# Performance work log

Hardware: AMD Instinct MI355X
Metric: run time of the kernel (lower is better)

Reference implementation:

```python
import jax, jax.numpy as jnp
import numpy as np

H = 1024        # hidden_size
NH = 16         # num_attention_heads
DH = H // NH    # head dim = 64
I = 4096        # intermediate_size
E = 8           # moe_num_experts
B, S = 2, 2048
EPS = 1e-12


def _ln(x, g, b):
    mu = jnp.mean(x, axis=-1, keepdims=True)
    var = jnp.mean(jnp.square(x - mu), axis=-1, keepdims=True)
    return (x - mu) * jax.lax.rsqrt(var + EPS) * g + b


def setup_inputs() -> dict:
    key = jax.random.key(0)
    ks = jax.random.split(key, 16)
    std = 0.02
    p = {
        "hidden_states": jax.random.normal(ks[0], (B, S, H), jnp.float32),
        "Wq": jax.random.normal(ks[1], (H, H), jnp.float32) * std,
        "bq": jnp.zeros((H,), jnp.float32),
        "Wk": jax.random.normal(ks[2], (H, H), jnp.float32) * std,
        "bk": jnp.zeros((H,), jnp.float32),
        "Wv": jax.random.normal(ks[3], (H, H), jnp.float32) * std,
        "bv": jnp.zeros((H,), jnp.float32),
        "Wao": jax.random.normal(ks[4], (H, H), jnp.float32) * std,
        "bao": jnp.zeros((H,), jnp.float32),
        "ln1_g": jnp.ones((H,), jnp.float32),
        "ln1_b": jnp.zeros((H,), jnp.float32),
        "router_w": jax.random.normal(ks[5], (H, E), jnp.float32) * std,
        "We": jax.random.normal(ks[6], (E, H, I), jnp.float32) * std,
        "be": jnp.zeros((E, I), jnp.float32),
        "Wo": jax.random.normal(ks[7], (I, H), jnp.float32) * std,
        "bo": jnp.zeros((H,), jnp.float32),
        "ln2_g": jnp.ones((H,), jnp.float32),
        "ln2_b": jnp.zeros((H,), jnp.float32),
    }
    return p


def reference(hidden_states, Wq, bq, Wk, bk, Wv, bv, Wao, bao, ln1_g, ln1_b,
              router_w, We, be, Wo, bo, ln2_g, ln2_b):
    x = hidden_states  # [B,S,H]

    def heads(t):  # [B,S,H] -> [B,NH,S,DH]
        return t.reshape(B, S, NH, DH).transpose(0, 2, 1, 3)

    q = heads(x @ Wq + bq)
    k = heads(x @ Wk + bk)
    v = heads(x @ Wv + bv)
    scores = jnp.einsum("bhqd,bhkd->bhqk", q, k) / jnp.sqrt(jnp.float32(DH))
    probs = jax.nn.softmax(scores, axis=-1)
    ctx = jnp.einsum("bhqk,bhkd->bhqd", probs, v)
    ctx = ctx.transpose(0, 2, 1, 3).reshape(B, S, H)
    attn_out = _ln(ctx @ Wao + bao + x, ln1_g, ln1_b)  # BertSelfOutput

    # ---- MoE FFN: top-1 routing, per-expert GELU MLP, shared output proj ----
    flat = attn_out.reshape(-1, H)              # [N,H]
    logits = flat @ router_w                    # [N,E]
    idx = jnp.argmax(logits, axis=-1)           # top-1 of softmax == argmax of logits
    inter = jnp.zeros((flat.shape[0], I), flat.dtype)
    for e in range(E):  # small fixed expert count
        h_e = jax.nn.gelu(flat @ We[e] + be[e], approximate=False)
        inter = jnp.where((idx == e)[:, None], h_e, inter)
    inter = inter.reshape(B, S, I)
    out = _ln(inter @ Wo + bo + attn_out, ln2_g, ln2_b)  # BertOutput
    return out
```

## Files before the change

kernel.cpp:

```cpp
#include <hip/hip_runtime.h>
#include <hip/hip_bf16.h>
#include <cstdint>

#define H_  1024
#define NH_ 16
#define DH_ 64
#define I_  4096
#define E_  8
#define B_  2
#define S_  2048
#define N_  4096
#define QKVLD 3072
#define LN_EPS 1e-12f

typedef __attribute__((ext_vector_type(4))) float f4;
typedef __attribute__((ext_vector_type(8))) short s8v;
typedef unsigned int u32;

__device__ __forceinline__ float bf2f(unsigned short u) {
  union { unsigned int i; float f; } c; c.i = ((unsigned int)u) << 16; return c.f;
}
__device__ __forceinline__ unsigned short f2bf(float f) {
  __hip_bfloat16 h = __float2bfloat16(f);
  return *reinterpret_cast<unsigned short*>(&h);
}
__device__ __forceinline__ u32 pack_bf2(float a, float b) {
  return (u32)f2bf(a) | ((u32)f2bf(b) << 16);
}
__device__ __forceinline__ float gelu_f(float x) {
  return 0.5f * x * (1.0f + erff(x * 0.70710678118f));
}
__device__ __forceinline__ void gload16(const void* g, void* l) {
  __builtin_amdgcn_global_load_lds(
      (const __attribute__((address_space(1))) void*)g,
      (__attribute__((address_space(3))) void*)l, 16, 0, 0);
}

__global__ __launch_bounds__(256) void cvt_bf16_kernel(
    const float* __restrict__ in, ushort* __restrict__ out, int n8)
{
  const int t = blockIdx.x * 256 + threadIdx.x;
  if (t >= n8) return;
  const f4 x0 = *(const f4*)(in + (size_t)t * 8);
  const f4 x1 = *(const f4*)(in + (size_t)t * 8 + 4);
  s8v o;
#pragma unroll
  for (int j = 0; j < 4; ++j) { o[j] = (short)f2bf(x0[j]); o[4 + j] = (short)f2bf(x1[j]); }
  *(s8v*)(out + (size_t)t * 8) = o;
}

__global__ __launch_bounds__(256) void transpose_cvt_kernel(
    const float* __restrict__ in, ushort* __restrict__ out, int R, int C)
{
  __shared__ float Ls[64][68];
  const size_t zo = (size_t)blockIdx.z * (size_t)R * C;
  const int bx = blockIdx.x << 6;
  const int by = blockIdx.y << 6;
  const int tid = threadIdx.x;
  const int lr = tid >> 4, lc4 = (tid & 15) << 2;
  const float* ip = in + zo + (size_t)(by + lr) * C + bx + lc4;
#pragma unroll
  for (int i = 0; i < 4; ++i)
    *(f4*)&Ls[lr + (i << 4)][lc4] = *(const f4*)(ip + (size_t)(i << 4) * C);
  __syncthreads();
  const int oc = tid >> 2, seg = (tid & 3) << 4;
  ushort* op = out + zo + (size_t)(bx + oc) * R + by + seg;
  s8v v0, v1;
#pragma unroll
  for (int j = 0; j < 8; ++j) {
    v0[j] = (short)f2bf(Ls[seg + j][oc]);
    v1[j] = (short)f2bf(Ls[seg + 8 + j][oc]);
  }
  *(s8v*)op = v0;
  *(s8v*)(op + 8) = v1;
}

__global__ void concat3_kernel(const float* a, const float* b, const float* c,
                               float* __restrict__ o)
{
  const int t = blockIdx.x * 256 + threadIdx.x;
  if (t < 1024) o[t] = a[t];
  else if (t < 2048) o[t] = b[t - 1024];
  else o[t] = c[t - 2048];
}

__global__ __launch_bounds__(256) void gather_kernel(
    const ushort* __restrict__ X, const int* __restrict__ lists,
    ushort* __restrict__ Xg)
{
  const int r = (blockIdx.x << 1) + (threadIdx.x >> 7);
  const int c = (threadIdx.x & 127) << 3;
  const int tok = lists[r];
  *(s8v*)&Xg[(size_t)r * H_ + c] = *(const s8v*)&X[(size_t)tok * H_ + c];
}

template <bool BF16OUT, int KSPLIT>
__global__ __launch_bounds__(256, 3) void gemm_mfma_kernel(
    const ushort* __restrict__ A, const ushort* __restrict__ Bt,
    const float* __restrict__ bias, void* __restrict__ Cout,
    const int M, const int N, const int K)
{
  __shared__ __align__(16) ushort Asm[3][4][128][8];
  __shared__ __align__(16) ushort Bsm[3][4][128][8];
  const int tid = threadIdx.x;
  const int w = tid >> 6, l = tid & 63;
  const int lq = l & 15, g = l >> 4;
  const int wm = w >> 1, wn = w & 1;
  const int nbx = N >> 7;
  const int nwg = nbx * (M >> 7);
  int id = blockIdx.y * nbx + blockIdx.x;
  id = (id & 7) * (nwg >> 3) + (id >> 3);
  const int m0 = (id / nbx) << 7, n0 = (id % nbx) << 7;
  const int Kspan = K / KSPLIT;
  const int kbase = (KSPLIT > 1) ? blockIdx.z * Kspan : 0;

  const ushort* a0 = A + (size_t)(m0 + l) * K + kbase + (w << 3);
  const ushort* a1 = a0 + (size_t)64 * K;
  const ushort* b0 = Bt + (size_t)(n0 + l) * K + kbase + (w << 3);
  const ushort* b1 = b0 + (size_t)64 * K;

  f4 acc[4][4] = {};
  const int nt = Kspan >> 5;
#define STAGE_G(tt, buf)                                   \
  { const int kt_ = (tt) << 5;                             \
    gload16(a0 + kt_, &Asm[buf][w][0][0]);                 \
    gload16(a1 + kt_, &Asm[buf][w][64][0]);                \
    gload16(b0 + kt_, &Bsm[buf][w][0][0]);                 \
    gload16(b1 + kt_, &Bsm[buf][w][64][0]); }
  STAGE_G(0, 0);
  STAGE_G(1, 1);
  int cur = 0, nxt2 = 2;
  for (int t = 0; t < nt; ++t) {
    if (t + 1 < nt) { asm volatile("s_waitcnt vmcnt(4)" ::: "memory"); }
    else            { asm volatile("s_waitcnt vmcnt(0)" ::: "memory"); }
    __builtin_amdgcn_s_barrier();
    __builtin_amdgcn_sched_barrier(0);
    if (t + 2 < nt) STAGE_G(t + 2, nxt2);
    s8v af[4], bfv[4];
#pragma unroll
    for (int mi = 0; mi < 4; ++mi)
      af[mi] = *(const s8v*)&Asm[cur][g][(wm << 6) + (mi << 4) + lq][0];
#pragma unroll
    for (int ni = 0; ni < 4; ++ni)
      bfv[ni] = *(const s8v*)&Bsm[cur][g][(wn << 6) + (ni << 4) + lq][0];
    asm volatile("s_waitcnt lgkmcnt(0)" ::: "memory");
    __builtin_amdgcn_sched_barrier(0);
#pragma unroll
    for (int mi = 0; mi < 4; ++mi)
#pragma unroll
      for (int ni = 0; ni < 4; ++ni)
        acc[mi][ni] = __builtin_amdgcn_mfma_f32_16x16x32_bf16(af[mi], bfv[ni], acc[mi][ni], 0, 0, 0);
    cur = (cur == 2) ? 0 : cur + 1;
    nxt2 = (nxt2 == 2) ? 0 : nxt2 + 1;
  }
#undef STAGE_G
  if constexpr (BF16OUT) {
    ushort* st = (ushort*)Asm + (size_t)w * (16 * 72);
    float bs[4];
#pragma unroll
    for (int ni = 0; ni < 4; ++ni) bs[ni] = bias[n0 + (wn << 6) + (ni << 4) + lq];
#pragma unroll
    for (int mi = 0; mi < 4; ++mi) {
#pragma unroll
      for (int ni = 0; ni < 4; ++ni)
#pragma unroll
        for (int r = 0; r < 4; ++r)
          st[((g << 2) + r) * 72 + (ni << 4) + lq] = f2bf(acc[mi][ni][r] + bs[ni]);
#pragma unroll
      for (int q2 = 0; q2 < 2; ++q2) {
        const int r16 = l & 15, ch = (l >> 4) + (q2 << 2);
        const s8v vv = *(const s8v*)&st[r16 * 72 + (ch << 3)];
        *(s8v*)&((ushort*)Cout)[(size_t)(m0 + (wm << 6) + (mi << 4) + r16) * N
                                + n0 + (wn << 6) + (ch << 3)] = vv;
      }
    }
  } else {
    float* outf = (float*)Cout + (size_t)blockIdx.z * M * N;
#pragma unroll
    for (int ni = 0; ni < 4; ++ni) {
      const int col = n0 + (wn << 6) + (ni << 4) + lq;
      const float bs = (KSPLIT == 1 || blockIdx.z == 0) ? bias[col] : 0.f;
#pragma unroll
      for (int mi = 0; mi < 4; ++mi) {
        const int row = m0 + (wm << 6) + (mi << 4) + (g << 2);
#pragma unroll
        for (int r = 0; r < 4; ++r)
          outf[(size_t)(row + r) * N + col] = acc[mi][ni][r] + bs;
      }
    }
  }
}

__global__ __launch_bounds__(256, 3) void moe_mfma_kernel(
    const ushort* __restrict__ Xg, const ushort* __restrict__ WeT,
    const float* __restrict__ be, const int* __restrict__ lists,
    const int* __restrict__ offs, const int* __restrict__ cnt,
    const int* __restrict__ tb, ushort* __restrict__ inter)
{
  __shared__ __align__(16) ushort Asm[3][4][128][8];
  __shared__ __align__(16) ushort Bsm[3][4][128][8];
  __shared__ int tokL[128];
  const int by = blockIdx.y;
  if (by >= tb[E_]) return;
  int e = 0;
#pragma unroll
  for (int t = 1; t < E_; ++t) if (by >= tb[t]) e = t;
  const int rt = by - tb[e];
  const int base = offs[e] + (rt << 7);
  const int nrows = cnt[e] - (rt << 7);
  const int tid = threadIdx.x;
  if (tid < 128) tokL[tid] = (tid < nrows) ? lists[base + tid] : -1;
  __syncthreads();
  const int w = tid >> 6, l = tid & 63;
  const int lq = l & 15, g = l >> 4;
  const int wm = w >> 1, wn = w & 1;
  const int n0 = blockIdx.x << 7;
  const int r0 = min(base + l, N_ - 1);
  const int r1 = min(base + 64 + l, N_ - 1);
  const ushort* a0 = Xg + (size_t)r0 * H_ + (w << 3);
  const ushort* a1 = Xg + (size_t)r1 * H_ + (w << 3);
  const ushort* Wp = WeT + (size_t)e * I_ * H_;
  const ushort* b0 = Wp + (size_t)(n0 + l) * H_ + (w << 3);
  const ushort* b1 = b0 + (size_t)64 * H_;

  f4 acc[4][4] = {};
#define STAGE_M(tt, buf)                                   \
  { const int kt_ = (tt) << 5;                             \
    gload16(a0 + kt_, &Asm[buf][w][0][0]);                 \
    gload16(a1 + kt_, &Asm[buf][w][64][0]);                \
    gload16(b0 + kt_, &Bsm[buf][w][0][0]);                 \
    gload16(b1 + kt_, &Bsm[buf][w][64][0]); }
  STAGE_M(0, 0);
  STAGE_M(1, 1);
  int cur = 0, nxt2 = 2;
  for (int t = 0; t < 32; ++t) {
    if (t + 1 < 32) { asm volatile("s_waitcnt vmcnt(4)" ::: "memory"); }
    else            { asm volatile("s_waitcnt vmcnt(0)" ::: "memory"); }
    __builtin_amdgcn_s_barrier();
    __builtin_amdgcn_sched_barrier(0);
    if (t + 2 < 32) STAGE_M(t + 2, nxt2);
    s8v af[4], bfv[4];
#pragma unroll
    for (int mi = 0; mi < 4; ++mi)
      af[mi] = *(const s8v*)&Asm[cur][g][(wm << 6) + (mi << 4) + lq][0];
#pragma unroll
    for (int ni = 0; ni < 4; ++ni)
      bfv[ni] = *(const s8v*)&Bsm[cur][g][(wn << 6) + (ni << 4) + lq][0];
    asm volatile("s_waitcnt lgkmcnt(0)" ::: "memory");
    __builtin_amdgcn_sched_barrier(0);
#pragma unroll
    for (int mi = 0; mi < 4; ++mi)
#pragma unroll
      for (int ni = 0; ni < 4; ++ni)
        acc[mi][ni] = __builtin_amdgcn_mfma_f32_16x16x32_bf16(af[mi], bfv[ni], acc[mi][ni], 0, 0, 0);
    cur = (cur == 2) ? 0 : cur + 1;
    nxt2 = (nxt2 == 2) ? 0 : nxt2 + 1;
  }
#undef STAGE_M
  {
    ushort* st = (ushort*)Asm + (size_t)w * (16 * 72);
    float bs[4];
#pragma unroll
    for (int ni = 0; ni < 4; ++ni) bs[ni] = be[(size_t)e * I_ + n0 + (wn << 6) + (ni << 4) + lq];
#pragma unroll
    for (int mi = 0; mi < 4; ++mi) {
#pragma unroll
      for (int ni = 0; ni < 4; ++ni)
#pragma unroll
        for (int r = 0; r < 4; ++r)
          st[((g << 2) + r) * 72 + (ni << 4) + lq] = f2bf(gelu_f(acc[mi][ni][r] + bs[ni]));
#pragma unroll
      for (int q2 = 0; q2 < 2; ++q2) {
        const int r16 = l & 15, ch = (l >> 4) + (q2 << 2);
        const int tok = tokL[(wm << 6) + (mi << 4) + r16];
        if (tok >= 0) {
          const s8v vv = *(const s8v*)&st[r16 * 72 + (ch << 3)];
          *(s8v*)&inter[(size_t)tok * I_ + n0 + (wn << 6) + (ch << 3)] = vv;
        }
      }
    }
  }
}

__global__ __launch_bounds__(256) void attn_mfma_kernel(
    const ushort* __restrict__ qkv, ushort* __restrict__ ctx)
{
  __shared__ __align__(16) ushort Ks[64 * 72];
  __shared__ __align__(16) ushort Vr[64 * 72];
  __shared__ __align__(16) ushort Vt[64 * 72];
  __shared__ __align__(16) ushort Ps[4][16 * 72];
  const int bid0 = blockIdx.x;
  const int bid  = ((bid0 & 7) << 7) + (bid0 >> 3);
  const int bh = bid >> 5, qt = bid & 31;
  const int b = bh >> 4, h = bh & 15;
  const int tid = threadIdx.x, w = tid >> 6, l = tid & 63;
  const int lq = l & 15, g = l >> 4;
  const size_t bS = (size_t)b * S_;
  const ushort* qb = qkv + bS * QKVLD + h * DH_;
  const ushort* kb = qb + 1024;
  const ushort* vb = qb + 2048;

  s8v qf0, qf1;
  {
    const ushort* qp = qb + (size_t)(qt * 64 + w * 16 + lq) * QKVLD;
    qf0 = *(const s8v*)(qp + (g << 3));
    qf1 = *(const s8v*)(qp + 32 + (g << 3));
  }

  f4 o0 = {0,0,0,0}, o1 = {0,0,0,0}, o2 = {0,0,0,0}, o3 = {0,0,0,0};
  float mrun = -3.0e38f, lrun = 0.f;

  const int skey = tid >> 2;
  const int sd   = (tid & 3) << 4;

  s8v kr0, kr1, vr0, vr1;
#define ALOAD(t_) {                                                        \
    const ushort* kp_ = kb + (size_t)((t_) * 64 + skey) * QKVLD + sd;      \
    kr0 = *(const s8v*)kp_; kr1 = *(const s8v*)(kp_ + 8);                  \
    const ushort* vp_ = vb + (size_t)((t_) * 64 + skey) * QKVLD + sd;      \
    vr0 = *(const s8v*)vp_; vr1 = *(const s8v*)(vp_ + 8); }
#define AWRITE() {                                                         \
    *(s8v*)&Ks[skey * 72 + sd]     = kr0;                                  \
    *(s8v*)&Ks[skey * 72 + sd + 8] = kr1;                                  \
    *(s8v*)&Vr[skey * 72 + sd]     = vr0;                                  \
    *(s8v*)&Vr[skey * 72 + sd + 8] = vr1; }

  ALOAD(0); AWRITE();
  ALOAD(1);

  for (int kt = 0; kt < 32; ++kt) {
    asm volatile("s_waitcnt lgkmcnt(0)" ::: "memory");
    __builtin_amdgcn_sched_barrier(0);
    __builtin_amdgcn_s_barrier();
    __builtin_amdgcn_sched_barrier(0);

    {
      s8v t0, t1;
#pragma unroll
      for (int j = 0; j < 8; ++j) {
        t0[j] = (short)Vr[(w * 16 + j) * 72 + l];
        t1[j] = (short)Vr[(w * 16 + 8 + j) * 72 + l];
      }
      *(s8v*)&Vt[l * 72 + w * 16]     = t0;
      *(s8v*)&Vt[l * 72 + w * 16 + 8] = t1;
    }

    float s[16];
    __builtin_amdgcn_s_setprio(1);
#pragma unroll
    for (int st = 0; st < 4; ++st) {
      f4 acc = {0, 0, 0, 0};
      const s8v ka0 = *(const s8v*)&Ks[(st * 16 + lq) * 72 + (g << 3)];
      const s8v ka1 = *(const s8v*)&Ks[(st * 16 + lq) * 72 + 32 + (g << 3)];
      acc = __builtin_amdgcn_mfma_f32_16x16x32_bf16(ka0, qf0, acc, 0, 0, 0);
      acc = __builtin_amdgcn_mfma_f32_16x16x32_bf16(ka1, qf1, acc, 0, 0, 0);
      s[st * 4 + 0] = acc[0] * 0.125f; s[st * 4 + 1] = acc[1] * 0.125f;
      s[st * 4 + 2] = acc[2] * 0.125f; s[st * 4 + 3] = acc[3] * 0.125f;
    }
    __builtin_amdgcn_s_setprio(0);

    float tmax = s[0];
// ... 56 lines not shown
  for (int r = 0; r < 4; ++r) {
    const float li = __shfl(inv, g * 4 + r);
    ushort* op = ctx + (bS + (size_t)(qt * 64 + w * 16 + g * 4 + r)) * H_ + h * DH_ + lq;
    op[0]  = f2bf(o0[r] * li);
    op[16] = f2bf(o1[r] * li);
    op[32] = f2bf(o2[r] * li);
    op[48] = f2bf(o3[r] * li);
  }
}

template <int P>
__global__ __launch_bounds__(256) void add_ln_kernel(
    const float* __restrict__ a, const float* __restrict__ r,
    const float* __restrict__ g, const float* __restrict__ bta,
    float* __restrict__ out, ushort* __restrict__ ob)
{
  const int row = blockIdx.x, tid = threadIdx.x;
  const size_t base = (size_t)row * H_;
  const float4 xr = *(const float4*)(r + base + (tid << 2));
  float4 x = xr;
#pragma unroll
  for (int pp = 0; pp < P; ++pp) {
    const float4 xa = *(const float4*)(a + (size_t)pp * N_ * H_ + base + (tid << 2));
    x.x += xa.x; x.y += xa.y; x.z += xa.z; x.w += xa.w;
  }
  float s  = x.x + x.y + x.z + x.w;
  float ss = x.x * x.x + x.y * x.y + x.z * x.z + x.w * x.w;
#pragma unroll
  for (int off = 1; off < 64; off <<= 1) { s += __shfl_xor(s, off); ss += __shfl_xor(ss, off); }
  __shared__ float red[8];
  const int w = tid >> 6, ln = tid & 63;
  if (ln == 0) { red[w] = s; red[4 + w] = ss; }
  __syncthreads();
  const float S  = red[0] + red[1] + red[2] + red[3];
  const float SS = red[4] + red[5] + red[6] + red[7];
  const float mu  = S * (1.f / 1024.f);
  const float var = fmaxf(SS * (1.f / 1024.f) - mu * mu, 0.f);
  const float inv = rsqrtf(var + LN_EPS);
  const float4 gg = *(const float4*)&g[tid << 2];
  const float4 bb = *(const float4*)&bta[tid << 2];
  float4 y;
  y.x = (x.x - mu) * inv * gg.x + bb.x;
  y.y = (x.y - mu) * inv * gg.y + bb.y;
  y.z = (x.z - mu) * inv * gg.z + bb.z;
  y.w = (x.w - mu) * inv * gg.w + bb.w;
  *(float4*)&out[base + (tid << 2)] = y;
  if (ob) {
    ushort4 u;
    u.x = f2bf(y.x); u.y = f2bf(y.y); u.z = f2bf(y.z); u.w = f2bf(y.w);
    *(ushort4*)&ob[base + (tid << 2)] = u;
  }
}

__global__ __launch_bounds__(64) void router_kernel(
    const float* __restrict__ x, const float* __restrict__ rw,
    int* __restrict__ idx, int* __restrict__ cnt)
{
  const int t = blockIdx.x, lane = threadIdx.x;
  float acc[8] = {0.f};
  for (int c = 0; c < H_; c += 64) {
    const float xv = x[(size_t)t * H_ + c + lane];
    const float* wr = rw + (size_t)(c + lane) * E_;
    const float4 w0 = *(const float4*)wr;
    const float4 w1 = *(const float4*)(wr + 4);
    acc[0] += xv * w0.x; acc[1] += xv * w0.y; acc[2] += xv * w0.z; acc[3] += xv * w0.w;
    acc[4] += xv * w1.x; acc[5] += xv * w1.y; acc[6] += xv * w1.z; acc[7] += xv * w1.w;
  }
#pragma unroll
  for (int e = 0; e < E_; ++e) {
    float s = acc[e];
#pragma unroll
    for (int off = 1; off < 64; off <<= 1) s += __shfl_xor(s, off);
    acc[e] = s;
  }
  if (lane == 0) {
    int be_ = 0; float bv = acc[0];
#pragma unroll
    for (int e = 1; e < E_; ++e) if (acc[e] > bv) { bv = acc[e]; be_ = e; }
    idx[t] = be_;
    atomicAdd(&cnt[be_], 1);
  }
}

__global__ void init_kernel(int* cnt) { if (threadIdx.x < E_) cnt[threadIdx.x] = 0; }

__global__ void scan_kernel(const int* __restrict__ cnt, int* __restrict__ offs,
                            int* __restrict__ cursor, int* __restrict__ tb)
{
  int o = 0, tt = 0;
  for (int e = 0; e < E_; ++e) {
    offs[e] = o; cursor[e] = o; tb[e] = tt;
    o += cnt[e]; tt += (cnt[e] + 127) >> 7;
  }
  tb[E_] = tt;
}

__global__ __launch_bounds__(256) void scatter_kernel(
    const int* __restrict__ idx, int* __restrict__ cursor, int* __restrict__ lists)
{
  const int t = blockIdx.x * 256 + threadIdx.x;
  if (t < N_) {
    const int e = idx[t];
    const int p = atomicAdd(&cursor[e], 1);
    lists[p] = t;
  }
}

extern "C" void kernel_launch(void* const* d_in, const int* in_sizes, int n_in,
                              void* d_out, int out_size, void* d_ws, size_t ws_size,
                              hipStream_t stream) {
  const float* x   = (const float*)d_in[0];
  const float* Wq  = (const float*)d_in[1];
  const float* bq  = (const float*)d_in[2];
  const float* Wk  = (const float*)d_in[3];
  const float* bk  = (const float*)d_in[4];
  const float* Wv  = (const float*)d_in[5];
  const float* bv  = (const float*)d_in[6];
  const float* Wao = (const float*)d_in[7];
  const float* bao = (const float*)d_in[8];
  const float* g1  = (const float*)d_in[9];
  const float* b1  = (const float*)d_in[10];
  const float* rw  = (const float*)d_in[11];
  const float* We  = (const float*)d_in[12];
  const float* be  = (const float*)d_in[13];
  const float* Wo  = (const float*)d_in[14];
  const float* bo  = (const float*)d_in[15];
  const float* g2  = (const float*)d_in[16];
  const float* b2  = (const float*)d_in[17];
  float* out = (float*)d_out;

  char* p = (char*)d_ws;
  int* idx    = (int*)p; p += (size_t)N_ * 4;
  int* cnt    = (int*)p; p += 8 * 4;
  int* offs   = (int*)p; p += 8 * 4;
  int* cursor = (int*)p; p += 8 * 4;
  int* tb     = (int*)p; p += 16 * 4;
  int* lists  = (int*)p; p += (size_t)N_ * 4;
  p = (char*)(((uintptr_t)p + 255) & ~(uintptr_t)255);
  const size_t NH = (size_t)N_ * H_;
  ushort* xb     = (ushort*)p; p += NH * 2;
  ushort* qkvb   = (ushort*)p;
  float*  woPart = (float*)p;  p += (size_t)N_ * QKVLD * 2;
  ushort* ctxb   = (ushort*)p; p += NH * 2;
  float*  attn   = (float*)p;  p += NH * 4;
  ushort* attnb  = (ushort*)p; p += NH * 2;
  ushort* interb = (ushort*)p;
  float*  aoPart = (float*)p;  p += (size_t)N_ * I_ * 2;
  ushort* WqkvT  = (ushort*)p; p += (size_t)QKVLD * H_ * 2;
  ushort* WaoT   = (ushort*)p; p += (size_t)H_ * H_ * 2;
  ushort* WoT    = (ushort*)p; p += (size_t)H_ * I_ * 2;
  ushort* WeT    = (ushort*)p; p += (size_t)E_ * I_ * H_ * 2;
  float*  bqkv   = (float*)p;  p += QKVLD * 4;
  ushort* Xg     = xb;

  const dim3 blk(256);

  init_kernel<<<1, 64, 0, stream>>>(cnt);
  cvt_bf16_kernel<<<(N_ * H_ / 8 + 255) / 256, blk, 0, stream>>>(x, xb, N_ * H_ / 8);
  concat3_kernel<<<QKVLD / 256, blk, 0, stream>>>(bq, bk, bv, bqkv);
  transpose_cvt_kernel<<<dim3(16, 16, 1), blk, 0, stream>>>(Wq, WqkvT, H_, H_);
  transpose_cvt_kernel<<<dim3(16, 16, 1), blk, 0, stream>>>(Wk, WqkvT + (size_t)1024 * H_, H_, H_);
  transpose_cvt_kernel<<<dim3(16, 16, 1), blk, 0, stream>>>(Wv, WqkvT + (size_t)2048 * H_, H_, H_);
  transpose_cvt_kernel<<<dim3(16, 16, 1), blk, 0, stream>>>(Wao, WaoT, H_, H_);
  transpose_cvt_kernel<<<dim3(16, 64, 1), blk, 0, stream>>>(Wo, WoT, I_, H_);
  transpose_cvt_kernel<<<dim3(64, 16, 8), blk, 0, stream>>>(We, WeT, H_, I_);

  gemm_mfma_kernel<true, 1><<<dim3(QKVLD / 128, N_ / 128), blk, 0, stream>>>(
      xb, WqkvT, bqkv, qkvb, N_, QKVLD, H_);
  attn_mfma_kernel<<<1024, blk, 0, stream>>>(qkvb, ctxb);
  gemm_mfma_kernel<false, 2><<<dim3(H_ / 128, N_ / 128, 2), blk, 0, stream>>>(
      ctxb, WaoT, bao, aoPart, N_, H_, H_);
  add_ln_kernel<2><<<N_, blk, 0, stream>>>(aoPart, x, g1, b1, attn, attnb);
  router_kernel<<<N_, 64, 0, stream>>>(attn, rw, idx, cnt);
  scan_kernel<<<1, 1, 0, stream>>>(cnt, offs, cursor, tb);
  scatter_kernel<<<N_ / 256, blk, 0, stream>>>(idx, cursor, lists);
  gather_kernel<<<N_ / 2, blk, 0, stream>>>(attnb, lists, Xg);
  moe_mfma_kernel<<<dim3(I_ / 128, N_ / 128 + E_), blk, 0, stream>>>(
      Xg, WeT, be, lists, offs, cnt, tb, interb);
  gemm_mfma_kernel<false, 2><<<dim3(H_ / 128, N_ / 128, 2), blk, 0, stream>>>(
      interb, WoT, bo, woPart, N_, H_, I_);
  add_ln_kernel<2><<<N_, blk, 0, stream>>>(woPart, attn, g2, b2, out, (ushort*)nullptr);
}
```

Before: 509.8 us.

## Use 256x256 tiles with 512-thread blocks for QKV and MoE expert GEMMs

Measured after the change: 506.2 us. About the same (-0.7%).

```diff
diff --git a/kernel.cpp b/kernel.cpp
--- a/kernel.cpp
+++ b/kernel.cpp
@@ -92,6 +92,185 @@
   const int c = (threadIdx.x & 127) << 3;
   const int tok = lists[r];
   *(s8v*)&Xg[(size_t)r * H_ + c] = *(const s8v*)&X[(size_t)tok * H_ + c];
+}
+
+__global__ __launch_bounds__(512, 2) void gemm256_bf16_kernel(
+    const ushort* __restrict__ A, const ushort* __restrict__ Bt,
+    const float* __restrict__ bias, ushort* __restrict__ Cout,
+    const int M, const int N, const int K)
+{
+  __shared__ __align__(16) ushort Asm[3][4][256][8];
+  __shared__ __align__(16) ushort Bsm[3][4][256][8];
+  const int tid = threadIdx.x, w = tid >> 6, l = tid & 63;
+  const int lq = l & 15, g = l >> 4;
+  const int wm = w >> 2, wn = w & 3;
+  const int nbx = N >> 8;
+  const int nwg = nbx * (M >> 8);
+  int id = blockIdx.y * nbx + blockIdx.x;
+  id = (id & 7) * (nwg >> 3) + (id >> 3);
+  const int m0 = (id / nbx) << 8, n0 = (id % nbx) << 8;
+
+  const bool isB = (w >= 4);
+  const int ks = w & 3;
+  const ushort* gb = isB ? (Bt + (size_t)(n0 + l) * K + (ks << 3))
+                         : (A + (size_t)(m0 + l) * K + (ks << 3));
+  const ushort* p0 = gb;
+  const ushort* p1 = gb + (size_t)64 * K;
+  const ushort* p2 = gb + (size_t)128 * K;
+  const ushort* p3 = gb + (size_t)192 * K;
+
+  f4 acc[8][4] = {};
+  const int nt = K >> 5;
+#define STG(tt, buf) { const int kt_ = (tt) << 5;                          \
+    ushort* d = isB ? &Bsm[buf][ks][0][0] : &Asm[buf][ks][0][0];           \
+    gload16(p0 + kt_, d);          gload16(p1 + kt_, d + 64 * 8);          \
+    gload16(p2 + kt_, d + 128 * 8); gload16(p3 + kt_, d + 192 * 8); }
+  STG(0, 0);
+  STG(1, 1);
+  int cur = 0, nxt2 = 2;
+  for (int t = 0; t < nt; ++t) {
+    if (t + 1 < nt) { asm volatile("s_waitcnt vmcnt(4)" ::: "memory"); }
+    else            { asm volatile("s_waitcnt vmcnt(0)" ::: "memory"); }
+    __builtin_amdgcn_s_barrier();
+    __builtin_amdgcn_sched_barrier(0);
+    if (t + 2 < nt) STG(t + 2, nxt2);
+    s8v af[8], bfv[4];
+#pragma unroll
+    for (int mi = 0; mi < 8; ++mi)
+      af[mi] = *(const s8v*)&Asm[cur][g][(wm << 7) + (mi << 4) + lq][0];
+#pragma unroll
+    for (int ni = 0; ni < 4; ++ni)
+      bfv[ni] = *(const s8v*)&Bsm[cur][g][(wn << 6) + (ni << 4) + lq][0];
+    asm volatile("s_waitcnt lgkmcnt(0)" ::: "memory");
+    __builtin_amdgcn_sched_barrier(0);
+#pragma unroll
+    for (int mi = 0; mi < 8; ++mi)
+#pragma unroll
+      for (int ni = 0; ni < 4; ++ni)
+        acc[mi][ni] = __builtin_amdgcn_mfma_f32_16x16x32_bf16(af[mi], bfv[ni], acc[mi][ni], 0, 0, 0);
+    cur = (cur == 2) ? 0 : cur + 1;
+    nxt2 = (nxt2 == 2) ? 0 : nxt2 + 1;
+  }
+#undef STG
+  __syncthreads();
+  ushort* st = (ushort*)Asm + (size_t)w * (16 * 72);
+  float bs[4];
+#pragma unroll
+  for (int ni = 0; ni < 4; ++ni) bs[ni] = bias[n0 + (wn << 6) + (ni << 4) + lq];
+#pragma unroll
+  for (int mi = 0; mi < 8; ++mi) {
+#pragma unroll
+    for (int ni = 0; ni < 4; ++ni)
+#pragma unroll
+      for (int r = 0; r < 4; ++r)
+        st[((g << 2) + r) * 72 + (ni << 4) + lq] = f2bf(acc[mi][ni][r] + bs[ni]);
+#pragma unroll
+    for (int q2 = 0; q2 < 2; ++q2) {
+      const int r16 = l & 15, ch = (l >> 4) + (q2 << 2);
+      const s8v vv = *(const s8v*)&st[r16 * 72 + (ch << 3)];
+      *(s8v*)&Cout[(size_t)(m0 + (wm << 7) + (mi << 4) + r16) * N
+                   + n0 + (wn << 6) + (ch << 3)] = vv;
+    }
+  }
+}
+
+__global__ __launch_bounds__(512, 2) void moe256_mfma_kernel(
+    const ushort* __restrict__ Xg, const ushort* __restrict__ WeT,
+    const float* __restrict__ be, const int* __restrict__ lists,
+    const int* __restrict__ offs, const int* __restrict__ cnt,
+    const int* __restrict__ tb, ushort* __restrict__ inter)
+{
+  __shared__ __align__(16) ushort Asm[3][4][256][8];
+  __shared__ __align__(16) ushort Bsm[3][4][256][8];
+  __shared__ int tokL[256];
+  const int by = blockIdx.y;
+  if (by >= tb[E_]) return;
+  int e = 0;
+#pragma unroll
+  for (int t = 1; t < E_; ++t) if (by >= tb[t]) e = t;
+  const int rt = by - tb[e];
+  const int base = offs[e] + (rt << 8);
+  const int nrows = cnt[e] - (rt << 8);
+  const int tid = threadIdx.x;
+  if (tid < 256) tokL[tid] = (tid < nrows) ? lists[base + tid] : -1;
+  __syncthreads();
+  const int w = tid >> 6, l = tid & 63;
+  const int lq = l & 15, g = l >> 4;
+  const int wm = w >> 2, wn = w & 3;
+  const int n0 = blockIdx.x << 8;
+
+  const bool isB = (w >= 4);
+  const int ks = w & 3;
+  const ushort* Wp = WeT + (size_t)e * I_ * H_;
+  const ushort* p0;
+  const ushort* p1;
+  const ushort* p2;
+  const ushort* p3;
+  if (isB) {
+    const ushort* gb = Wp + (size_t)(n0 + l) * H_ + (ks << 3);
+    p0 = gb; p1 = gb + (size_t)64 * H_; p2 = gb + (size_t)128 * H_; p3 = gb + (size_t)192 * H_;
+  } else {
+    p0 = Xg + (size_t)min(base + l,       N_ - 1) * H_ + (ks << 3);
+    p1 = Xg + (size_t)min(base + 64 + l,  N_ - 1) * H_ + (ks << 3);
+    p2 = Xg + (size_t)min(base + 128 + l, N_ - 1) * H_ + (ks << 3);
+    p3 = Xg + (size_t)min(base + 192 + l, N_ - 1) * H_ + (ks << 3);
+  }
+
+  f4 acc[8][4] = {};
+#define STG(tt, buf) { const int kt_ = (tt) << 5;                          \
+    ushort* d = isB ? &Bsm[buf][ks][0][0] : &Asm[buf][ks][0][0];           \
+    gload16(p0 + kt_, d);          gload16(p1 + kt_, d + 64 * 8);          \
+    gload16(p2 + kt_, d + 128 * 8); gload16(p3 + kt_, d + 192 * 8); }
+  STG(0, 0);
+  STG(1, 1);
+  int cur = 0, nxt2 = 2;
+  for (int t = 0; t < 32; ++t) {
+    if (t + 1 < 32) { asm volatile("s_waitcnt vmcnt(4)" ::: "memory"); }
+    else            { asm volatile("s_waitcnt vmcnt(0)" ::: "memory"); }
+    __builtin_amdgcn_s_barrier();
+    __builtin_amdgcn_sched_barrier(0);
+    if (t + 2 < 32) STG(t + 2, nxt2);
+    s8v af[8], bfv[4];
+#pragma unroll
+    for (int mi = 0; mi < 8; ++mi)
+      af[mi] = *(const s8v*)&Asm[cur][g][(wm << 7) + (mi << 4) + lq][0];
+#pragma unroll
+    for (int ni = 0; ni < 4; ++ni)
+      bfv[ni] = *(const s8v*)&Bsm[cur][g][(wn << 6) + (ni << 4) + lq][0];
+    asm volatile("s_waitcnt lgkmcnt(0)" ::: "memory");
+    __builtin_amdgcn_sched_barrier(0);
+#pragma unroll
+    for (int mi = 0; mi < 8; ++mi)
+#pragma unroll
+      for (int ni = 0; ni < 4; ++ni)
+        acc[mi][ni] = __builtin_amdgcn_mfma_f32_16x16x32_bf16(af[mi], bfv[ni], acc[mi][ni], 0, 0, 0);
+    cur = (cur == 2) ? 0 : cur + 1;
+    nxt2 = (nxt2 == 2) ? 0 : nxt2 + 1;
+  }
+#undef STG
+  __syncthreads();
+  ushort* st = (ushort*)Asm + (size_t)w * (16 * 72);
+  float bs[4];
+#pragma unroll
+  for (int ni = 0; ni < 4; ++ni)
+    bs[ni] = be[(size_t)e * I_ + n0 + (wn << 6) + (ni << 4) + lq];
+#pragma unroll
+  for (int mi = 0; mi < 8; ++mi) {
+#pragma unroll
+    for (int ni = 0; ni < 4; ++ni)
+#pragma unroll
+      for (int r = 0; r < 4; ++r)
+        st[((g << 2) + r) * 72 + (ni << 4) + lq] = f2bf(gelu_f(acc[mi][ni][r] + bs[ni]));
+#pragma unroll
+    for (int q2 = 0; q2 < 2; ++q2) {
+      const int r16 = l & 15, ch = (l >> 4) + (q2 << 2);
+      const int tok = tokL[(wm << 7) + (mi << 4) + r16];
+      if (tok >= 0) {
+        const s8v vv = *(const s8v*)&st[r16 * 72 + (ch << 3)];
+        *(s8v*)&inter[(size_t)tok * I_ + n0 + (wn << 6) + (ch << 3)] = vv;
+      }
+    }
+  }
 }
 
 template <bool BF16OUT, int KSPLIT>
@@ -155,6 +334,7 @@
   }
 #undef STAGE_G
   if constexpr (BF16OUT) {
+    __syncthreads();
     ushort* st = (ushort*)Asm + (size_t)w * (16 * 72);
     float bs[4];
 #pragma unroll
@@ -186,97 +366,6 @@
 #pragma unroll
         for (int r = 0; r < 4; ++r)
           outf[(size_t)(row + r) * N + col] = acc[mi][ni][r] + bs;
-      }
-    }
-  }
-}
-
-__global__ __launch_bounds__(256, 3) void moe_mfma_kernel(
-    const ushort* __restrict__ Xg, const ushort* __restrict__ WeT,
-    const float* __restrict__ be, const int* __restrict__ lists,
-    const int* __restrict__ offs, const int* __restrict__ cnt,
-    const int* __restrict__ tb, ushort* __restrict__ inter)
-{
-  __shared__ __align__(16) ushort Asm[3][4][128][8];
-  __shared__ __align__(16) ushort Bsm[3][4][128][8];
-  __shared__ int tokL[128];
-  const int by = blockIdx.y;
-  if (by >= tb[E_]) return;
-  int e = 0;
-#pragma unroll
-  for (int t = 1; t < E_; ++t) if (by >= tb[t]) e = t;
-  const int rt = by - tb[e];
-  const int base = offs[e] + (rt << 7);
-  const int nrows = cnt[e] - (rt << 7);
-  const int tid = threadIdx.x;
-  if (tid < 128) tokL[tid] = (tid < nrows) ? lists[base + tid] : -1;
-  __syncthreads();
-  const int w = tid >> 6, l = tid & 63;
-  const int lq = l & 15, g = l >> 4;
-  const int wm = w >> 1, wn = w & 1;
-  const int n0 = blockIdx.x << 7;
-  const int r0 = min(base + l, N_ - 1);
-  const int r1 = min(base + 64 + l, N_ - 1);
-  const ushort* a0 = Xg + (size_t)r0 * H_ + (w << 3);
-  const ushort* a1 = Xg + (size_t)r1 * H_ + (w << 3);
-  const ushort* Wp = WeT + (size_t)e * I_ * H_;
-  const ushort* b0 = Wp + (size_t)(n0 + l) * H_ + (w << 3);
-  const ushort* b1 = b0 + (size_t)64 * H_;
-
-  f4 acc[4][4] = {};
-#define STAGE_M(tt, buf)                                   \
-  { const int kt_ = (tt) << 5;                             \
-    gload16(a0 + kt_, &Asm[buf][w][0][0]);                 \
-    gload16(a1 + kt_, &Asm[buf][w][64][0]);                \
-    gload16(b0 + kt_, &Bsm[buf][w][0][0]);                 \
-    gload16(b1 + kt_, &Bsm[buf][w][64][0]); }
-  STAGE_M(0, 0);
-  STAGE_M(1, 1);
-  int cur = 0, nxt2 = 2;
-  for (int t = 0; t < 32; ++t) {
-    if (t + 1 < 32) { asm volatile("s_waitcnt vmcnt(4)" ::: "memory"); }
-    else            { asm volatile("s_waitcnt vmcnt(0)" ::: "memory"); }
-    __builtin_amdgcn_s_barrier();
-    __builtin_amdgcn_sched_barrier(0);
-    if (t + 2 < 32) STAGE_M(t + 2, nxt2);
-    s8v af[4], bfv[4];
-#pragma unroll
-    for (int mi = 0; mi < 4; ++mi)
-      af[mi] = *(const s8v*)&Asm[cur][g][(wm << 6) + (mi << 4) + lq][0];
-#pragma unroll
-    for (int ni = 0; ni < 4; ++ni)
-      bfv[ni] = *(const s8v*)&Bsm[cur][g][(wn << 6) + (ni << 4) + lq][0];
-    asm volatile("s_waitcnt lgkmcnt(0)" ::: "memory");
-    __builtin_amdgcn_sched_barrier(0);
-#pragma unroll
-    for (int mi = 0; mi < 4; ++mi)
-#pragma unroll
-      for (int ni = 0; ni < 4; ++ni)
-        acc[mi][ni] = __builtin_amdgcn_mfma_f32_16x16x32_bf16(af[mi], bfv[ni], acc[mi][ni], 0, 0, 0);
-    cur = (cur == 2) ? 0 : cur + 1;
-    nxt2 = (nxt2 == 2) ? 0 : nxt2 + 1;
-  }
-#undef STAGE_M
-  {
-    ushort* st = (ushort*)Asm + (size_t)w * (16 * 72);
-    float bs[4];
-#pragma unroll
-    for (int ni = 0; ni < 4; ++ni) bs[ni] = be[(size_t)e * I_ + n0 + (wn << 6) + (ni << 4) + lq];
-#pragma unroll
-    for (int mi = 0; mi < 4; ++mi) {
-#pragma unroll
-      for (int ni = 0; ni < 4; ++ni)
-#pragma unroll
-        for (int r = 0; r < 4; ++r)
-          st[((g << 2) + r) * 72 + (ni << 4) + lq] = f2bf(gelu_f(acc[mi][ni][r] + bs[ni]));
-#pragma unroll
-      for (int q2 = 0; q2 < 2; ++q2) {
-        const int r16 = l & 15, ch = (l >> 4) + (q2 << 2);
-        const int tok = tokL[(wm << 6) + (mi << 4) + r16];
-        if (tok >= 0) {
-          const s8v vv = *(const s8v*)&st[r16 * 72 + (ch << 3)];
-          *(s8v*)&inter[(size_t)tok * I_ + n0 + (wn << 6) + (ch << 3)] = vv;
-        }
       }
     }
   }
@@ -507,7 +596,7 @@
   int o = 0, tt = 0;
   for (int e = 0; e < E_; ++e) {
     offs[e] = o; cursor[e] = o; tb[e] = tt;
-    o += cnt[e]; tt += (cnt[e] + 127) >> 7;
+    o += cnt[e]; tt += (cnt[e] + 255) >> 8;
   }
   tb[E_] = tt;
 }
@@ -582,7 +671,7 @@
   transpose_cvt_kernel<<<dim3(16, 64, 1), blk, 0, stream>>>(Wo, WoT, I_, H_);
   transpose_cvt_kernel<<<dim3(64, 16, 8), blk, 0, stream>>>(We, WeT, H_, I_);
 
-  gemm_mfma_kernel<true, 1><<<dim3(QKVLD / 128, N_ / 128), blk, 0, stream>>>(
+  gemm256_bf16_kernel<<<dim3(QKVLD / 256, N_ / 256), dim3(512), 0, stream>>>(
       xb, WqkvT, bqkv, qkvb, N_, QKVLD, H_);
   attn_mfma_kernel<<<1024, blk, 0, stream>>>(qkvb, ctxb);
   gemm_mfma_kernel<false, 2><<<dim3(H_ / 128, N_ / 128, 2), blk, 0, stream>>>(
@@ -592,7 +681,7 @@
   scan_kernel<<<1, 1, 0, stream>>>(cnt, offs, cursor, tb);
   scatter_kernel<<<N_ / 256, blk, 0, stream>>>(idx, cursor, lists);
   gather_kernel<<<N_ / 2, blk, 0, stream>>>(attnb, lists, Xg);
-  moe_mfma_kernel<<<dim3(I_ / 128, N_ / 128 + E_), blk, 0, stream>>>(
+  moe256_mfma_kernel<<<dim3(I_ / 256, N_ / 256 + E_), dim3(512), 0, stream>>>(
       Xg, WeT, be, lists, offs, cnt, tb, interb);
   gemm_mfma_kernel<false, 2><<<dim3(H_ / 128, N_ / 128, 2), blk, 0, stream>>>(
       interb, WoT, bo, woPart, N_, H_, I_);
```

## Load GEMM fragments directly from global into registers, dropping LDS staging

Applied to the files above, without the earlier changes.

Measured after the change: 648.6 us. +27.2%, slower.

```diff
diff --git a/kernel.cpp b/kernel.cpp
--- a/kernel.cpp
+++ b/kernel.cpp
@@ -30,11 +30,6 @@
 __device__ __forceinline__ float gelu_f(float x) {
   return 0.5f * x * (1.0f + erff(x * 0.70710678118f));
 }
-__device__ __forceinline__ void gload16(const void* g, void* l) {
-  __builtin_amdgcn_global_load_lds(
-      (const __attribute__((address_space(1))) void*)g,
-      (__attribute__((address_space(3))) void*)l, 16, 0, 0);
-}
 
 __global__ __launch_bounds__(256) void cvt_bf16_kernel(
     const float* __restrict__ in, ushort* __restrict__ out, int n8)
@@ -95,13 +90,12 @@
 }
 
 template <bool BF16OUT, int KSPLIT>
-__global__ __launch_bounds__(256, 3) void gemm_mfma_kernel(
+__global__ __launch_bounds__(256, 3) void gemm_dg_kernel(
     const ushort* __restrict__ A, const ushort* __restrict__ Bt,
     const float* __restrict__ bias, void* __restrict__ Cout,
     const int M, const int N, const int K)
 {
-  __shared__ __align__(16) ushort Asm[3][4][128][8];
-  __shared__ __align__(16) ushort Bsm[3][4][128][8];
+  __shared__ __align__(16) ushort st4[4][16 * 72];
   const int tid = threadIdx.x;
   const int w = tid >> 6, l = tid & 63;
   const int lq = l & 15, g = l >> 4;
@@ -114,48 +108,43 @@
   const int Kspan = K / KSPLIT;
   const int kbase = (KSPLIT > 1) ? blockIdx.z * Kspan : 0;
 
-  const ushort* a0 = A + (size_t)(m0 + l) * K + kbase + (w << 3);
-  const ushort* a1 = a0 + (size_t)64 * K;
-  const ushort* b0 = Bt + (size_t)(n0 + l) * K + kbase + (w << 3);
-  const ushort* b1 = b0 + (size_t)64 * K;
+  const ushort* ap[4];
+  const ushort* bp[4];
+#pragma unroll
+  for (int mi = 0; mi < 4; ++mi)
+    ap[mi] = A + (size_t)(m0 + (wm << 6) + (mi << 4) + lq) * K + kbase + (g << 3);
+#pragma unroll
+  for (int ni = 0; ni < 4; ++ni)
+    bp[ni] = Bt + (size_t)(n0 + (wn << 6) + (ni << 4) + lq) * K + kbase + (g << 3);
 
   f4 acc[4][4] = {};
   const int nt = Kspan >> 5;
-#define STAGE_G(tt, buf)                                   \
-  { const int kt_ = (tt) << 5;                             \
-    gload16(a0 + kt_, &Asm[buf][w][0][0]);                 \
-    gload16(a1 + kt_, &Asm[buf][w][64][0]);                \
-    gload16(b0 + kt_, &Bsm[buf][w][0][0]);                 \
-    gload16(b1 + kt_, &Bsm[buf][w][64][0]); }
-  STAGE_G(0, 0);
-  STAGE_G(1, 1);
-  int cur = 0, nxt2 = 2;
+  s8v a0[4], b0[4], a1[4], b1[4];
+#pragma unroll
+  for (int mi = 0; mi < 4; ++mi) a0[mi] = *(const s8v*)(ap[mi]);
+#pragma unroll
+  for (int ni = 0; ni < 4; ++ni) b0[ni] = *(const s8v*)(bp[ni]);
+#pragma unroll 2
   for (int t = 0; t < nt; ++t) {
-    if (t + 1 < nt) { asm volatile("s_waitcnt vmcnt(4)" ::: "memory"); }
-    else            { asm volatile("s_waitcnt vmcnt(0)" ::: "memory"); }
-    __builtin_amdgcn_s_barrier();
-    __builtin_amdgcn_sched_barrier(0);
-    if (t + 2 < nt) STAGE_G(t + 2, nxt2);
-    s8v af[4], bfv[4];
+    if (t + 1 < nt) {
+      const int kt = (t + 1) << 5;
+#pragma unroll
+      for (int mi = 0; mi < 4; ++mi) a1[mi] = *(const s8v*)(ap[mi] + kt);
+#pragma unroll
+      for (int ni = 0; ni < 4; ++ni) b1[ni] = *(const s8v*)(bp[ni] + kt);
+    }
 #pragma unroll
     for (int mi = 0; mi < 4; ++mi)
-      af[mi] = *(const s8v*)&Asm[cur][g][(wm << 6) + (mi << 4) + lq][0];
-#pragma unroll
-    for (int ni = 0; ni < 4; ++ni)
-      bfv[ni] = *(const s8v*)&Bsm[cur][g][(wn << 6) + (ni << 4) + lq][0];
-    asm volatile("s_waitcnt lgkmcnt(0)" ::: "memory");
-    __builtin_amdgcn_sched_barrier(0);
-#pragma unroll
-    for (int mi = 0; mi < 4; ++mi)
 #pragma unroll
       for (int ni = 0; ni < 4; ++ni)
-        acc[mi][ni] = __builtin_amdgcn_mfma_f32_16x16x32_bf16(af[mi], bfv[ni], acc[mi][ni], 0, 0, 0);
-    cur = (cur == 2) ? 0 : cur + 1;
-    nxt2 = (nxt2 == 2) ? 0 : nxt2 + 1;
-  }
-#undef STAGE_G
+        acc[mi][ni] = __builtin_amdgcn_mfma_f32_16x16x32_bf16(a0[mi], b0[ni], acc[mi][ni], 0, 0, 0);
+#pragma unroll
+    for (int mi = 0; mi < 4; ++mi) a0[mi] = a1[mi];
+#pragma unroll
+    for (int ni = 0; ni < 4; ++ni) b0[ni] = b1[ni];
+  }
   if constexpr (BF16OUT) {
-    ushort* st = (ushort*)Asm + (size_t)w * (16 * 72);
+    ushort* st = &st4[w][0];
     float bs[4];
 #pragma unroll
     for (int ni = 0; ni < 4; ++ni) bs[ni] = bias[n0 + (wn << 6) + (ni << 4) + lq];
@@ -191,14 +180,13 @@
   }
 }
 
-__global__ __launch_bounds__(256, 3) void moe_mfma_kernel(
+__global__ __launch_bounds__(256, 3) void moe_dg_kernel(
     const ushort* __restrict__ Xg, const ushort* __restrict__ WeT,
     const float* __restrict__ be, const int* __restrict__ lists,
     const int* __restrict__ offs, const int* __restrict__ cnt,
     const int* __restrict__ tb, ushort* __restrict__ inter)
 {
-  __shared__ __align__(16) ushort Asm[3][4][128][8];
-  __shared__ __align__(16) ushort Bsm[3][4][128][8];
+  __shared__ __align__(16) ushort st4[4][16 * 72];
   __shared__ int tokL[128];
   const int by = blockIdx.y;
   if (by >= tb[E_]) return;
@@ -215,53 +203,50 @@
   const int lq = l & 15, g = l >> 4;
   const int wm = w >> 1, wn = w & 1;
   const int n0 = blockIdx.x << 7;
-  const int r0 = min(base + l, N_ - 1);
-  const int r1 = min(base + 64 + l, N_ - 1);
-  const ushort* a0 = Xg + (size_t)r0 * H_ + (w << 3);
-  const ushort* a1 = Xg + (size_t)r1 * H_ + (w << 3);
+
+  const ushort* ap[4];
+  const ushort* bp[4];
+#pragma unroll
+  for (int mi = 0; mi < 4; ++mi) {
+    const int ridx = min(base + (wm << 6) + (mi << 4) + lq, N_ - 1);
+    ap[mi] = Xg + (size_t)ridx * H_ + (g << 3);
+  }
   const ushort* Wp = WeT + (size_t)e * I_ * H_;
-  const ushort* b0 = Wp + (size_t)(n0 + l) * H_ + (w << 3);
-  const ushort* b1 = b0 + (size_t)64 * H_;
+#pragma unroll
+  for (int ni = 0; ni < 4; ++ni)
+    bp[ni] = Wp + (size_t)(n0 + (wn << 6) + (ni << 4) + lq) * H_ + (g << 3);
 
   f4 acc[4][4] = {};
-#define STAGE_M(tt, buf)                                   \
-  { const int kt_ = (tt) << 5;                             \
-    gload16(a0 + kt_, &Asm[buf][w][0][0]);                 \
-    gload16(a1 + kt_, &Asm[buf][w][64][0]);                \
-    gload16(b0 + kt_, &Bsm[buf][w][0][0]);                 \
-    gload16(b1 + kt_, &Bsm[buf][w][64][0]); }
-  STAGE_M(0, 0);
-  STAGE_M(1, 1);
-  int cur = 0, nxt2 = 2;
+  s8v a0[4], b0[4], a1[4], b1[4];
+#pragma unroll
+  for (int mi = 0; mi < 4; ++mi) a0[mi] = *(const s8v*)(ap[mi]);
+#pragma unroll
+  for (int ni = 0; ni < 4; ++ni) b0[ni] = *(const s8v*)(bp[ni]);
+#pragma unroll 2
   for (int t = 0; t < 32; ++t) {
-    if (t + 1 < 32) { asm volatile("s_waitcnt vmcnt(4)" ::: "memory"); }
-    else            { asm volatile("s_waitcnt vmcnt(0)" ::: "memory"); }
-    __builtin_amdgcn_s_barrier();
-    __builtin_amdgcn_sched_barrier(0);
-    if (t + 2 < 32) STAGE_M(t + 2, nxt2);
-    s8v af[4], bfv[4];
+    if (t + 1 < 32) {
+      const int kt = (t + 1) << 5;
+#pragma unroll
+      for (int mi = 0; mi < 4; ++mi) a1[mi] = *(const s8v*)(ap[mi] + kt);
+#pragma unroll
+      for (int ni = 0; ni < 4; ++ni) b1[ni] = *(const s8v*)(bp[ni] + kt);
+    }
 #pragma unroll
     for (int mi = 0; mi < 4; ++mi)
-      af[mi] = *(const s8v*)&Asm[cur][g][(wm << 6) + (mi << 4) + lq][0];
+#pragma unroll
+      for (int ni = 0; ni < 4; ++ni)
+        acc[mi][ni] = __builtin_amdgcn_mfma_f32_16x16x32_bf16(a0[mi], b0[ni], acc[mi][ni], 0, 0, 0);
+#pragma unroll
+    for (int mi = 0; mi < 4; ++mi) a0[mi] = a1[mi];
+#pragma unroll
+    for (int ni = 0; ni < 4; ++ni) b0[ni] = b1[ni];
+  }
+  {
+    ushort* st = &st4[w][0];
+    float bs[4];
 #pragma unroll
     for (int ni = 0; ni < 4; ++ni)
-      bfv[ni] = *(const s8v*)&Bsm[cur][g][(wn << 6) + (ni << 4) + lq][0];
-    asm volatile("s_waitcnt lgkmcnt(0)" ::: "memory");
-    __builtin_amdgcn_sched_barrier(0);
-#pragma unroll
-    for (int mi = 0; mi < 4; ++mi)
-#pragma unroll
-      for (int ni = 0; ni < 4; ++ni)
-        acc[mi][ni] = __builtin_amdgcn_mfma_f32_16x16x32_bf16(af[mi], bfv[ni], acc[mi][ni], 0, 0, 0);
-    cur = (cur == 2) ? 0 : cur + 1;
-    nxt2 = (nxt2 == 2) ? 0 : nxt2 + 1;
-  }
-#undef STAGE_M
-  {
-    ushort* st = (ushort*)Asm + (size_t)w * (16 * 72);
-    float bs[4];
-#pragma unroll
-    for (int ni = 0; ni < 4; ++ni) bs[ni] = be[(size_t)e * I_ + n0 + (wn << 6) + (ni << 4) + lq];
+      bs[ni] = be[(size_t)e * I_ + n0 + (wn << 6) + (ni << 4) + lq];
 #pragma unroll
     for (int mi = 0; mi < 4; ++mi) {
 #pragma unroll
@@ -582,19 +567,19 @@
   transpose_cvt_kernel<<<dim3(16, 64, 1), blk, 0, stream>>>(Wo, WoT, I_, H_);
   transpose_cvt_kernel<<<dim3(64, 16, 8), blk, 0, stream>>>(We, WeT, H_, I_);
 
-  gemm_mfma_kernel<true, 1><<<dim3(QKVLD / 128, N_ / 128), blk, 0, stream>>>(
+  gemm_dg_kernel<true, 1><<<dim3(QKVLD / 128, N_ / 128), blk, 0, stream>>>(
       xb, WqkvT, bqkv, qkvb, N_, QKVLD, H_);
   attn_mfma_kernel<<<1024, blk, 0, stream>>>(qkvb, ctxb);
-  gemm_mfma_kernel<false, 2><<<dim3(H_ / 128, N_ / 128, 2), blk, 0, stream>>>(
+  gemm_dg_kernel<false, 2><<<dim3(H_ / 128, N_ / 128, 2), blk, 0, stream>>>(
       ctxb, WaoT, bao, aoPart, N_, H_, H_);
   add_ln_kernel<2><<<N_, blk, 0, stream>>>(aoPart, x, g1, b1, attn, attnb);
   router_kernel<<<N_, 64, 0, stream>>>(attn, rw, idx, cnt);
   scan_kernel<<<1, 1, 0, stream>>>(cnt, offs, cursor, tb);
   scatter_kernel<<<N_ / 256, blk, 0, stream>>>(idx, cursor, lists);
   gather_kernel<<<N_ / 2, blk, 0, stream>>>(attnb, lists, Xg);
-  moe_mfma_kernel<<<dim3(I_ / 128, N_ / 128 + E_), blk, 0, stream>>>(
+  moe_dg_kernel<<<dim3(I_ / 128, N_ / 128 + E_), blk, 0, stream>>>(
       Xg, WeT, be, lists, offs, cnt, tb, interb);
-  gemm_mfma_kernel<false, 2><<<dim3(H_ / 128, N_ / 128, 2), blk, 0, stream>>>(
+  gemm_dg_kernel<false, 2><<<dim3(H_ / 128, N_ / 128, 2), blk, 0, stream>>>(
       interb, WoT, bo, woPart, N_, H_, I_);
   add_ln_kernel<2><<<N_, blk, 0, stream>>>(woPart, attn, g2, b2, out, (ushort*)nullptr);
 }
```

## Deepen GEMM LDS pipeline to four stages and fuse small routing kernels

Applied to the files above, without the earlier changes.

After: 516.1 us. Within noise of the previous version (+1.2%).

```diff
diff --git a/kernel.cpp b/kernel.cpp
--- a/kernel.cpp
+++ b/kernel.cpp
@@ -37,8 +37,9 @@
 }
 
 __global__ __launch_bounds__(256) void cvt_bf16_kernel(
-    const float* __restrict__ in, ushort* __restrict__ out, int n8)
-{
+    const float* __restrict__ in, ushort* __restrict__ out, int n8, int* __restrict__ cnt)
+{
+  if (blockIdx.x == 0 && threadIdx.x < E_) cnt[threadIdx.x] = 0;
   const int t = blockIdx.x * 256 + threadIdx.x;
   if (t >= n8) return;
   const f4 x0 = *(const f4*)(in + (size_t)t * 8);
@@ -84,6 +85,28 @@
   else o[t] = c[t - 2048];
 }
 
+__global__ __launch_bounds__(256) void scan_scatter_kernel(
+    const int* __restrict__ idx, const int* __restrict__ cnt,
+    int* __restrict__ offs, int* __restrict__ tb, int* __restrict__ lists)
+{
+  __shared__ int lcur[E_];
+  const int tid = threadIdx.x;
+  if (tid == 0) {
+    int o = 0, tt = 0;
+    for (int e = 0; e < E_; ++e) {
+      offs[e] = o; lcur[e] = o; tb[e] = tt;
+      o += cnt[e]; tt += (cnt[e] + 127) >> 7;
+    }
+    tb[E_] = tt;
+  }
+  __syncthreads();
+  for (int t = tid; t < N_; t += 256) {
+    const int e = idx[t];
+    const int p = atomicAdd(&lcur[e], 1);
+    lists[p] = t;
+  }
+}
+
 __global__ __launch_bounds__(256) void gather_kernel(
     const ushort* __restrict__ X, const int* __restrict__ lists,
     ushort* __restrict__ Xg)
@@ -95,13 +118,13 @@
 }
 
 template <bool BF16OUT, int KSPLIT>
-__global__ __launch_bounds__(256, 3) void gemm_mfma_kernel(
+__global__ __launch_bounds__(256, 4) void gemm_mfma_kernel(
     const ushort* __restrict__ A, const ushort* __restrict__ Bt,
     const float* __restrict__ bias, void* __restrict__ Cout,
     const int M, const int N, const int K)
 {
-  __shared__ __align__(16) ushort Asm[3][4][128][8];
-  __shared__ __align__(16) ushort Bsm[3][4][128][8];
+  __shared__ __align__(16) ushort Asm[4][4][128][8];
+  __shared__ __align__(16) ushort Bsm[4][4][128][8];
   const int tid = threadIdx.x;
   const int w = tid >> 6, l = tid & 63;
   const int lq = l & 15, g = l >> 4;
@@ -129,13 +152,16 @@
     gload16(b1 + kt_, &Bsm[buf][w][64][0]); }
   STAGE_G(0, 0);
   STAGE_G(1, 1);
-  int cur = 0, nxt2 = 2;
+  STAGE_G(2, 2);
   for (int t = 0; t < nt; ++t) {
-    if (t + 1 < nt) { asm volatile("s_waitcnt vmcnt(4)" ::: "memory"); }
-    else            { asm volatile("s_waitcnt vmcnt(0)" ::: "memory"); }
+    const int cur = t & 3;
+    const int rem = nt - 1 - t;
+    if (rem >= 2)      { asm volatile("s_waitcnt vmcnt(8)" ::: "memory"); }
+    else if (rem == 1) { asm volatile("s_waitcnt vmcnt(4)" ::: "memory"); }
+    else               { asm volatile("s_waitcnt vmcnt(0)" ::: "memory"); }
     __builtin_amdgcn_s_barrier();
     __builtin_amdgcn_sched_barrier(0);
-    if (t + 2 < nt) STAGE_G(t + 2, nxt2);
+    if (t + 3 < nt) STAGE_G(t + 3, (t + 3) & 3);
     s8v af[4], bfv[4];
 #pragma unroll
     for (int mi = 0; mi < 4; ++mi)
@@ -150,11 +176,10 @@
 #pragma unroll
       for (int ni = 0; ni < 4; ++ni)
         acc[mi][ni] = __builtin_amdgcn_mfma_f32_16x16x32_bf16(af[mi], bfv[ni], acc[mi][ni], 0, 0, 0);
-    cur = (cur == 2) ? 0 : cur + 1;
-    nxt2 = (nxt2 == 2) ? 0 : nxt2 + 1;
   }
 #undef STAGE_G
   if constexpr (BF16OUT) {
+    __syncthreads();
     ushort* st = (ushort*)Asm + (size_t)w * (16 * 72);
     float bs[4];
 #pragma unroll
@@ -191,14 +216,14 @@
   }
 }
 
-__global__ __launch_bounds__(256, 3) void moe_mfma_kernel(
+__global__ __launch_bounds__(256, 4) void moe_mfma_kernel(
     const ushort* __restrict__ Xg, const ushort* __restrict__ WeT,
     const float* __restrict__ be, const int* __restrict__ lists,
     const int* __restrict__ offs, const int* __restrict__ cnt,
     const int* __restrict__ tb, ushort* __restrict__ inter)
 {
-  __shared__ __align__(16) ushort Asm[3][4][128][8];
-  __shared__ __align__(16) ushort Bsm[3][4][128][8];
+  __shared__ __align__(16) ushort Asm[4][4][128][8];
+  __shared__ __align__(16) ushort Bsm[4][4][128][8];
   __shared__ int tokL[128];
   const int by = blockIdx.y;
   if (by >= tb[E_]) return;
@@ -232,13 +257,16 @@
     gload16(b1 + kt_, &Bsm[buf][w][64][0]); }
   STAGE_M(0, 0);
   STAGE_M(1, 1);
-  int cur = 0, nxt2 = 2;
+  STAGE_M(2, 2);
   for (int t = 0; t < 32; ++t) {
-    if (t + 1 < 32) { asm volatile("s_waitcnt vmcnt(4)" ::: "memory"); }
-    else            { asm volatile("s_waitcnt vmcnt(0)" ::: "memory"); }
+    const int cur = t & 3;
+    const int rem = 31 - t;
+    if (rem >= 2)      { asm volatile("s_waitcnt vmcnt(8)" ::: "memory"); }
+    else if (rem == 1) { asm volatile("s_waitcnt vmcnt(4)" ::: "memory"); }
+    else               { asm volatile("s_waitcnt vmcnt(0)" ::: "memory"); }
     __builtin_amdgcn_s_barrier();
     __builtin_amdgcn_sched_barrier(0);
-    if (t + 2 < 32) STAGE_M(t + 2, nxt2);
+    if (t + 3 < 32) STAGE_M(t + 3, (t + 3) & 3);
     s8v af[4], bfv[4];
 #pragma unroll
     for (int mi = 0; mi < 4; ++mi)
@@ -253,10 +281,9 @@
 #pragma unroll
       for (int ni = 0; ni < 4; ++ni)
         acc[mi][ni] = __builtin_amdgcn_mfma_f32_16x16x32_bf16(af[mi], bfv[ni], acc[mi][ni], 0, 0, 0);
-    cur = (cur == 2) ? 0 : cur + 1;
-    nxt2 = (nxt2 == 2) ? 0 : nxt2 + 1;
   }
 #undef STAGE_M
+  __syncthreads();
   {
     ushort* st = (ushort*)Asm + (size_t)w * (16 * 72);
     float bs[4];
@@ -499,30 +526,6 @@
   }
 }
 
-__global__ void init_kernel(int* cnt) { if (threadIdx.x < E_) cnt[threadIdx.x] = 0; }
-
-__global__ void scan_kernel(const int* __restrict__ cnt, int* __restrict__ offs,
-                            int* __restrict__ cursor, int* __restrict__ tb)
-{
-  int o = 0, tt = 0;
-  for (int e = 0; e < E_; ++e) {
-    offs[e] = o; cursor[e] = o; tb[e] = tt;
-    o += cnt[e]; tt += (cnt[e] + 127) >> 7;
-  }
-  tb[E_] = tt;
-}
-
-__global__ __launch_bounds__(256) void scatter_kernel(
-    const int* __restrict__ idx, int* __restrict__ cursor, int* __restrict__ lists)
-{
-  const int t = blockIdx.x * 256 + threadIdx.x;
-  if (t < N_) {
-    const int e = idx[t];
-    const int p = atomicAdd(&cursor[e], 1);
-    lists[p] = t;
-  }
-}
-
 extern "C" void kernel_launch(void* const* d_in, const int* in_sizes, int n_in,
                               void* d_out, int out_size, void* d_ws, size_t ws_size,
                               hipStream_t stream) {
@@ -550,7 +553,6 @@
   int* idx    = (int*)p; p += (size_t)N_ * 4;
   int* cnt    = (int*)p; p += 8 * 4;
   int* offs   = (int*)p; p += 8 * 4;
-  int* cursor = (int*)p; p += 8 * 4;
   int* tb     = (int*)p; p += 16 * 4;
   int* lists  = (int*)p; p += (size_t)N_ * 4;
   p = (char*)(((uintptr_t)p + 255) & ~(uintptr_t)255);
@@ -572,8 +574,7 @@
 
   const dim3 blk(256);
 
-  init_kernel<<<1, 64, 0, stream>>>(cnt);
-  cvt_bf16_kernel<<<(N_ * H_ / 8 + 255) / 256, blk, 0, stream>>>(x, xb, N_ * H_ / 8);
+  cvt_bf16_kernel<<<(N_ * H_ / 8 + 255) / 256, blk, 0, stream>>>(x, xb, N_ * H_ / 8, cnt);
   concat3_kernel<<<QKVLD / 256, blk, 0, stream>>>(bq, bk, bv, bqkv);
   transpose_cvt_kernel<<<dim3(16, 16, 1), blk, 0, stream>>>(Wq, WqkvT, H_, H_);
   transpose_cvt_kernel<<<dim3(16, 16, 1), blk, 0, stream>>>(Wk, WqkvT + (size_t)1024 * H_, H_, H_);
@@ -589,8 +590,7 @@
       ctxb, WaoT, bao, aoPart, N_, H_, H_);
   add_ln_kernel<2><<<N_, blk, 0, stream>>>(aoPart, x, g1, b1, attn, attnb);
   router_kernel<<<N_, 64, 0, stream>>>(attn, rw, idx, cnt);
-  scan_kernel<<<1, 1, 0, stream>>>(cnt, offs, cursor, tb);
-  scatter_kernel<<<N_ / 256, blk, 0, stream>>>(idx, cursor, lists);
+  scan_scatter_kernel<<<1, blk, 0, stream>>>(idx, cnt, offs, tb, lists);
   gather_kernel<<<N_ / 2, blk, 0, stream>>>(attnb, lists, Xg);
   moe_mfma_kernel<<<dim3(I_ / 128, N_ / 128 + E_), blk, 0, stream>>>(
       Xg, WeT, be, lists, offs, cnt, tb, interb);
```
